# Kernel optimization log

Measured on AMD Instinct MI355X. Metric: run time of the kernel, lower is better.

## Reference

```python
import jax, jax.numpy as jnp
import numpy as np

D_IN, D_SAE, T, L, K = 2304, 2048, 4, 6, 128
B = 32


def setup_inputs() -> dict:
    key = jax.random.key(0)
    kx, ke, kd = jax.random.split(key, 3)
    x = jax.random.normal(kx, (B, T, L, D_IN), dtype=jnp.float32)
    W_enc = jax.random.normal(ke, (T, L, D_IN, D_SAE), dtype=jnp.float32) / np.sqrt(D_IN).astype(np.float32)
    W_dec = jax.random.normal(kd, (T, L, D_SAE, D_IN), dtype=jnp.float32) / np.sqrt(D_SAE).astype(np.float32)
    b_enc = jnp.zeros((D_SAE,), dtype=jnp.float32)
    b_dec = jnp.zeros((T, L, D_IN), dtype=jnp.float32)
    return {"x": x, "W_enc": W_enc, "W_dec": W_dec, "b_enc": b_enc, "b_dec": b_dec}


def reference(x, W_enc, W_dec, b_enc, b_dec):
    # encode: per-(t,l) matmul, pre: (B, T, L, d_sae)
    pre = jnp.einsum('btld,tlds->btls', x, W_enc) + b_enc
    Bn = pre.shape[0]
    pre_flat = pre.reshape(Bn, T * L * D_SAE)
    # global TopK over the whole (T, L, d_sae) latent grid
    v, idx = jax.lax.top_k(pre_flat, K)
    z_flat = jnp.zeros_like(pre_flat).at[jnp.arange(Bn)[:, None], idx].set(jax.nn.relu(v))
    z = z_flat.reshape(Bn, T, L, D_SAE)
    # decode: per-(t,l) matmul
    x_hat = jnp.einsum('btls,tlsd->btld', z, W_dec) + b_dec
    loss = jnp.mean(jnp.sum(jnp.square(x_hat - x), axis=-1))
    return (loss, x_hat, z)
```

## Files before the change

### kernel.cpp

```cpp
#include <hip/hip_runtime.h>

#define D_IN   2304
#define D_SAE  2048
#define TL     24
#define BATCH  32
#define K_TOP  128
#define NLAT   (TL * D_SAE)
#define NBIN   8192
#define CAP    2048
#define KSPLIT 2
#define KS     (D_IN / KSPLIT)
#define BK     32
#define NCH    (KS / BK)

typedef __attribute__((ext_vector_type(8))) short short8;
typedef __attribute__((ext_vector_type(4))) float f32x4;

__device__ __forceinline__ void async_cp16(const float* g, float* l) {
    __builtin_amdgcn_global_load_lds(
        (const __attribute__((address_space(1))) unsigned int*)g,
        (__attribute__((address_space(3))) unsigned int*)l, 16, 0, 0);
}

__device__ __forceinline__ void cvt8(const float* f, short8& hi, short8& lo) {
#pragma unroll
    for (int j = 0; j < 8; ++j) {
        unsigned u = __float_as_uint(f[j]);
        hi[j] = (short)(u >> 16);
        float l = f[j] - __uint_as_float(u & 0xFFFF0000u);
        lo[j] = (short)(__float_as_uint(l) >> 16);
    }
}

__global__ __launch_bounds__(256, 3) void enc_kernel(const float* __restrict__ x,
                                                     const float* __restrict__ W,
                                                     float* __restrict__ part) {
    __shared__ float w_s[2][BK][128];
    __shared__ float x_s[2][32][36];

    const int tid  = threadIdx.x;
    const int lane = tid & 63;
    const int wv   = tid >> 6;
    const int m0   = lane & 15;
    const int kb   = lane >> 4;
    const int tl   = blockIdx.y;
    const int ks   = blockIdx.z;
    const int n0b  = blockIdx.x * 128;
    const int kb0  = ks * KS;

    const float* Wbase = W + ((size_t)(tl * D_IN + kb0)) * D_SAE + n0b;
    const int xb = tid >> 3, xq = (tid & 7) * 4;
    const float* xsrc = x + ((size_t)(xb * TL + tl)) * D_IN + kb0 + xq;

#define STAGE_W(buf, ch)                                                        \
    do {                                                                        \
        const float* Wc = Wbase + (size_t)((ch) * BK) * D_SAE;                  \
        _Pragma("unroll")                                                       \
        for (int j = 0; j < 4; ++j) {                                           \
            int r = wv * 8 + j * 2;                                             \
            async_cp16(Wc + (size_t)(r + (lane >> 5)) * D_SAE + (lane & 31) * 4,\
                       &w_s[buf][r][0]);                                        \
        }                                                                       \
    } while (0)

    f32x4 acc[2][2];
#pragma unroll
    for (int mt = 0; mt < 2; ++mt)
#pragma unroll
        for (int nt = 0; nt < 2; ++nt) acc[mt][nt] = (f32x4)(0.f);

    {
        float4 xr = *(const float4*)xsrc;
        STAGE_W(0, 0);
        asm volatile("s_waitcnt vmcnt(0)" ::: "memory");
        *(float4*)&x_s[0][xb][xq] = xr;
        __syncthreads();
    }

    int cur = 0;
    for (int ch = 0; ch < NCH; ++ch) {
        float4 xr;
        if (ch + 1 < NCH) {
            xr = *(const float4*)(xsrc + (ch + 1) * BK);
            STAGE_W(cur ^ 1, ch + 1);
        }

        const float(*ws)[128] = w_s[cur];
        const float(*xs)[36]  = x_s[cur];
        short8 ahi[2], alo[2];
#pragma unroll
        for (int mt = 0; mt < 2; ++mt) {
            float xa[8];
            *(float4*)&xa[0] = *(const float4*)&xs[mt * 16 + m0][kb * 8];
            *(float4*)&xa[4] = *(const float4*)&xs[mt * 16 + m0][kb * 8 + 4];
            cvt8(xa, ahi[mt], alo[mt]);
        }
#pragma unroll
        for (int nt = 0; nt < 2; ++nt) {
            float wf[8];
#pragma unroll
            for (int j = 0; j < 8; ++j)
                wf[j] = ws[kb * 8 + j][wv * 32 + nt * 16 + m0];
            short8 bhi, blo;
            cvt8(wf, bhi, blo);
#pragma unroll
            for (int mt = 0; mt < 2; ++mt) {
                acc[mt][nt] = __builtin_amdgcn_mfma_f32_16x16x32_bf16(ahi[mt], bhi, acc[mt][nt], 0, 0, 0);
                acc[mt][nt] = __builtin_amdgcn_mfma_f32_16x16x32_bf16(ahi[mt], blo, acc[mt][nt], 0, 0, 0);
                acc[mt][nt] = __builtin_amdgcn_mfma_f32_16x16x32_bf16(alo[mt], bhi, acc[mt][nt], 0, 0, 0);
            }
        }

        if (ch + 1 < NCH) {
            asm volatile("s_waitcnt vmcnt(0)" ::: "memory");
            *(float4*)&x_s[cur ^ 1][xb][xq] = xr;
        }
        __syncthreads();
        cur ^= 1;
    }
#undef STAGE_W

    float* pp = part + ((size_t)ks * BATCH) * NLAT + (size_t)tl * D_SAE + n0b;
#pragma unroll
    for (int mt = 0; mt < 2; ++mt)
#pragma unroll
        for (int nt = 0; nt < 2; ++nt)
#pragma unroll
            for (int r = 0; r < 4; ++r)
                pp[(size_t)(mt * 16 + kb * 4 + r) * NLAT + wv * 32 + nt * 16 + m0] =
                    acc[mt][nt][r];
}

__global__ void reduce_kernel(const float* __restrict__ part,
                              const float* __restrict__ b_enc,
                              float* __restrict__ pre) {
    int i = (blockIdx.x * blockDim.x + threadIdx.x) * 4;
    const size_t S = (size_t)BATCH * NLAT;
    float4 v = *(const float4*)&b_enc[i & (D_SAE - 1)];
#pragma unroll
    for (int s = 0; s < KSPLIT; s++) {
        float4 p = *(const float4*)&part[i + s * S];
        v.x += p.x; v.y += p.y; v.z += p.z; v.w += p.w;
    }
    *(float4*)&pre[i] = v;
}

__global__ __launch_bounds__(256) void topk_kernel(const float* __restrict__ pre,
                                                   int* __restrict__ sel_idx,
                                                   float* __restrict__ sel_val,
                                                   float* __restrict__ z,
                                                   float* __restrict__ loss) {
    const int b   = blockIdx.x;
    const int tid = threadIdx.x;
    __shared__ unsigned hist[NBIN];
    __shared__ unsigned cand_key[CAP];
    __shared__ int      cand_idx[CAP];
    __shared__ unsigned tsum[256];
    __shared__ unsigned suf[256];
    __shared__ int s_T, s_hi, s_ccnt, s_sel;

    const float* row  = pre + (size_t)b * NLAT;
    float*       zrow = z   + (size_t)b * NLAT;
    for (int i = tid; i < NBIN; i += 256) hist[i] = 0;
    if (tid == 0) { s_ccnt = 0; s_sel = 0; if (b == 0) *loss = 0.f; }
    __syncthreads();

    for (int i = 4 * tid; i < NLAT; i += 1024) {
        float4 v = *(const float4*)&row[i];
#pragma unroll
        for (int j = 0; j < 4; j++) {
            unsigned u   = __float_as_uint(((const float*)&v)[j]);
            unsigned key = u ^ ((u >> 31) ? 0xFFFFFFFFu : 0x80000000u);
            atomicAdd(&hist[key >> 19], 1u);
        }
    }
    __syncthreads();

    unsigned local = 0;
    const int base = tid * (NBIN / 256);
    for (int j = 0; j < NBIN / 256; j++) local += hist[base + j];
    tsum[tid] = local;
    __syncthreads();
    if (tid == 0) {
        unsigned run = 0;
        for (int t = 255; t >= 0; t--) { suf[t] = run; run += tsum[t]; }
    }
    __syncthreads();
    if (suf[tid] < K_TOP && suf[tid] + tsum[tid] >= K_TOP) {
        unsigned c = suf[tid];
        for (int j = NBIN / 256 - 1; j >= 0; j--) {
            int bin = base + j;
            if (c + hist[bin] >= K_TOP) { s_T = bin; s_hi = (int)c; break; }
            c += hist[bin];
        }
    }
    __syncthreads();

    const int T = s_T;
    for (int i = 4 * tid; i < NLAT; i += 1024) {
        float4 v = *(const float4*)&row[i];
#pragma unroll
        for (int j = 0; j < 4; j++) {
            float f      = ((const float*)&v)[j];
            unsigned u   = __float_as_uint(f);
            unsigned key = u ^ ((u >> 31) ? 0xFFFFFFFFu : 0x80000000u);
            int bin      = (int)(key >> 19);
            float rl     = fmaxf(f, 0.f);
            float zval   = 0.f;
            if (bin > T) {
                int p = atomicAdd(&s_sel, 1);
                sel_idx[b * K_TOP + p] = i + j;
                sel_val[b * K_TOP + p] = rl;
                zval = rl;
            } else if (bin == T) {
                int p = atomicAdd(&s_ccnt, 1);
                if (p < CAP) { cand_key[p] = key; cand_idx[p] = i + j; }
            }
            zrow[i + j] = zval;
        }
    }
    __syncthreads();

    const int need = K_TOP - s_hi;
    const int nc   = min(s_ccnt, CAP);
    for (int c = tid; c < nc; c += 256) {
        unsigned kc = cand_key[c]; int ic = cand_idx[c];
        int rank = 0;
        for (int j = 0; j < nc; j++) {
            unsigned kj = cand_key[j]; int ij = cand_idx[j];
            rank += (kj > kc) || (kj == kc && ij < ic);
        }
        if (rank < need) {
            int p = atomicAdd(&s_sel, 1);
            float rl = fmaxf(row[ic], 0.f);
            sel_idx[b * K_TOP + p] = ic;
            sel_val[b * K_TOP + p] = rl;
            zrow[ic] = rl;
        }
    }
}

__global__ __launch_bounds__(256) void dec_kernel(const float* __restrict__ Wd,
                                                  const float* __restrict__ b_dec,
                                                  const float* __restrict__ x,
                                                  const int* __restrict__ sel_idx,
                                                  const float* __restrict__ sel_val,
                                                  float* __restrict__ xhat,
                                                  float* __restrict__ loss) {
    const int tl = blockIdx.x, b = blockIdx.y, tid = threadIdx.x;
    float acc[9];
#pragma unroll
    for (int r = 0; r < 9; r++) acc[r] = b_dec[tl * D_IN + tid + r * 256];

    __shared__ int   s_idx[K_TOP];
    __shared__ float s_val[K_TOP];
    if (tid < K_TOP) { s_idx[tid] = sel_idx[b * K_TOP + tid];
                       s_val[tid] = sel_val[b * K_TOP + tid]; }
    __syncthreads();

    for (int j = 0; j < K_TOP; j++) {
        int f = s_idx[j];
        if ((f >> 11) == tl) {
            float v = s_val[j];
            const float* wrow = Wd + (size_t)f * D_IN;
#pragma unroll
            for (int r = 0; r < 9; r++)
                acc[r] = fmaf(v, wrow[tid + r * 256], acc[r]);
        }
    }

    const float* xr = x    + ((size_t)b * TL + tl) * D_IN;
    float*       xo = xhat + ((size_t)b * TL + tl) * D_IN;
    float lsum = 0.f;
#pragma unroll
    for (int r = 0; r < 9; r++) {
        float d = acc[r] - xr[tid + r * 256];
        xo[tid + r * 256] = acc[r];
        lsum += d * d;
    }
    __shared__ float red[256];
    red[tid] = lsum; __syncthreads();
    for (int s = 128; s > 0; s >>= 1) {
        if (tid < s) red[tid] += red[tid + s];
        __syncthreads();
    }
    if (tid == 0) atomicAdd(loss, red[0] * (1.0f / (BATCH * TL)));
}

extern "C" void kernel_launch(void* const* d_in, const int* in_sizes, int n_in,
                              void* d_out, int out_size, void* d_ws, size_t ws_size,
                              hipStream_t stream) {
    const float* x     = (const float*)d_in[0];
    const float* W_enc = (const float*)d_in[1];
    const float* W_dec = (const float*)d_in[2];
    const float* b_enc = (const float*)d_in[3];
    const float* b_dec = (const float*)d_in[4];

    float* out  = (float*)d_out;
    float* loss = out;
    float* xhat = out + 1;
    float* z    = out + 1 + (size_t)BATCH * TL * D_IN;

    const size_t S = (size_t)BATCH * NLAT;
    float* part    = (float*)d_ws;
    float* pre     = part + (size_t)KSPLIT * S;
    int*   sel_idx = (int*)(pre + S);
    float* sel_val = (float*)(sel_idx + BATCH * K_TOP);

    enc_kernel<<<dim3(16, TL, KSPLIT), 256, 0, stream>>>(x, W_enc, part);
    reduce_kernel<<<(int)(S / 1024), 256, 0, stream>>>(part, b_enc, pre);
    topk_kernel<<<BATCH, 256, 0, stream>>>(pre, sel_idx, sel_val, z, loss);
    dec_kernel<<<dim3(TL, BATCH), 256, 0, stream>>>(W_dec, b_dec, x, sel_idx, sel_val,
                                                    xhat, loss);
}
```

Baseline: 167.2 us.

## Pre-transpose x, async-stage both operands, and move top-k histogram into reduce pass

Adds a transpose kernel that writes x in a swizzled per-(t,l) layout and also zeroes a global histogram and the loss. The encoder now loads both operands with async global-to-LDS copies, using XOR-swizzled columns to avoid bank conflicts, and its occupancy hint rises to 4. The reduce kernel now zeros z and builds per-row histograms with global atomics, so the top-k kernel skips one full pass over each row. Top-k runs with 512 threads and a parallel suffix scan instead of a serial one. The costs are an extra launch, extra workspace, and heavy global atomic contention on the histogram bins.

```diff
diff --git a/kernel.cpp b/kernel.cpp
--- a/kernel.cpp
+++ b/kernel.cpp
@@ -12,6 +12,7 @@
 #define KS     (D_IN / KSPLIT)
 #define BK     32
 #define NCH    (KS / BK)
+#define TOPK_T 512
 
 typedef __attribute__((ext_vector_type(8))) short short8;
 typedef __attribute__((ext_vector_type(4))) float f32x4;
@@ -32,11 +33,35 @@
     }
 }
 
-__global__ __launch_bounds__(256, 3) void enc_kernel(const float* __restrict__ x,
+__global__ __launch_bounds__(256) void xT_kernel(const float* __restrict__ x,
+                                                 float* __restrict__ xT,
+                                                 unsigned* __restrict__ ghist,
+                                                 float* __restrict__ loss) {
+    __shared__ float ts[32][257];
+    const int tl = blockIdx.y, k0 = blockIdx.x * 256, tid = threadIdx.x;
+#pragma unroll 4
+    for (int r = 0; r < 32; ++r)
+        ts[r][tid] = x[((size_t)(r * TL + tl)) * D_IN + k0 + tid];
+    __syncthreads();
+    const int bb = tid & 31, kq = tid >> 5;
+#pragma unroll 4
+    for (int jj = 0; jj < 32; ++jj) {
+        int kk = kq + jj * 8;
+        int kg = k0 + kk;
+        int pc = (bb + 8 * ((kg >> 3) & 3)) & 31;
+        xT[((size_t)tl * D_IN + kg) * 32 + pc] = ts[bb][kk];
+    }
+    int gid = (blockIdx.y * gridDim.x + blockIdx.x) * 256 + tid;
+    for (int i = gid; i < BATCH * NBIN / 4; i += 216 * 256)
+        ((uint4*)ghist)[i] = make_uint4(0, 0, 0, 0);
+    if (gid == 0) *loss = 0.f;
+}
+
+__global__ __launch_bounds__(256, 4) void enc_kernel(const float* __restrict__ xT,
                                                      const float* __restrict__ W,
                                                      float* __restrict__ part) {
     __shared__ float w_s[2][BK][128];
-    __shared__ float x_s[2][32][36];
+    __shared__ float x_s[2][BK][32];
 
     const int tid  = threadIdx.x;
     const int lane = tid & 63;
@@ -45,22 +70,28 @@
     const int kb   = lane >> 4;
     const int tl   = blockIdx.y;
     const int ks   = blockIdx.z;
-    const int n0b  = blockIdx.x * 128;
-    const int kb0  = ks * KS;
-
-    const float* Wbase = W + ((size_t)(tl * D_IN + kb0)) * D_SAE + n0b;
-    const int xb = tid >> 3, xq = (tid & 7) * 4;
-    const float* xsrc = x + ((size_t)(xb * TL + tl)) * D_IN + kb0 + xq;
-
-#define STAGE_W(buf, ch)                                                        \
+    const int col0 = blockIdx.x * 128;
+
+    const float* Wbase = W + ((size_t)(tl * D_IN + ks * KS)) * D_SAE + col0;
+    const float* xbase = xT + ((size_t)(tl * D_IN + ks * KS)) * 32;
+
+    int colp[2];
+#pragma unroll
+    for (int nt = 0; nt < 2; ++nt)
+        colp[nt] = ((((wv * 8 + nt * 4 + (m0 >> 2)) ^ kb)) << 2) | (m0 & 3);
+    const int c0 = (m0 + 8 * kb) & 31;
+    const int c1 = (m0 + 16 + 8 * kb) & 31;
+
+#define STAGE(BUF, CH)                                                          \
     do {                                                                        \
-        const float* Wc = Wbase + (size_t)((ch) * BK) * D_SAE;                  \
+        const float* Wc = Wbase + (size_t)(CH) * BK * D_SAE;                    \
         _Pragma("unroll")                                                       \
-        for (int j = 0; j < 4; ++j) {                                           \
-            int r = wv * 8 + j * 2;                                             \
-            async_cp16(Wc + (size_t)(r + (lane >> 5)) * D_SAE + (lane & 31) * 4,\
-                       &w_s[buf][r][0]);                                        \
-        }                                                                       \
+        for (int i = 0; i < 4; ++i)                                             \
+            async_cp16(Wc + (size_t)(wv * 8 + 2 * i + (lane >> 5)) * D_SAE      \
+                          + ((lane & 31) ^ wv) * 4,                             \
+                       &w_s[BUF][wv * 8 + 2 * i][0]);                           \
+        async_cp16(xbase + (CH) * 1024 + wv * 256 + lane * 4,                   \
+                   &x_s[BUF][wv * 8][0]);                                       \
     } while (0)
 
     f32x4 acc[2][2];
@@ -69,58 +100,48 @@
 #pragma unroll
         for (int nt = 0; nt < 2; ++nt) acc[mt][nt] = (f32x4)(0.f);
 
-    {
-        float4 xr = *(const float4*)xsrc;
-        STAGE_W(0, 0);
-        asm volatile("s_waitcnt vmcnt(0)" ::: "memory");
-        *(float4*)&x_s[0][xb][xq] = xr;
-        __syncthreads();
-    }
+    STAGE(0, 0);
+    asm volatile("s_waitcnt vmcnt(0)" ::: "memory");
+    __builtin_amdgcn_s_barrier();
 
     int cur = 0;
     for (int ch = 0; ch < NCH; ++ch) {
-        float4 xr;
-        if (ch + 1 < NCH) {
-            xr = *(const float4*)(xsrc + (ch + 1) * BK);
-            STAGE_W(cur ^ 1, ch + 1);
-        }
+        if (ch + 1 < NCH) STAGE(cur ^ 1, ch + 1);
 
         const float(*ws)[128] = w_s[cur];
-        const float(*xs)[36]  = x_s[cur];
-        short8 ahi[2], alo[2];
-#pragma unroll
-        for (int mt = 0; mt < 2; ++mt) {
+        const float(*xs)[32]  = x_s[cur];
+        short8 a0h, a0l, a1h, a1l;
+        {
             float xa[8];
-            *(float4*)&xa[0] = *(const float4*)&xs[mt * 16 + m0][kb * 8];
-            *(float4*)&xa[4] = *(const float4*)&xs[mt * 16 + m0][kb * 8 + 4];
-            cvt8(xa, ahi[mt], alo[mt]);
+#pragma unroll
+            for (int j = 0; j < 8; ++j) xa[j] = xs[kb * 8 + j][c0];
+            cvt8(xa, a0h, a0l);
+#pragma unroll
+            for (int j = 0; j < 8; ++j) xa[j] = xs[kb * 8 + j][c1];
+            cvt8(xa, a1h, a1l);
         }
 #pragma unroll
         for (int nt = 0; nt < 2; ++nt) {
             float wf[8];
 #pragma unroll
-            for (int j = 0; j < 8; ++j)
-                wf[j] = ws[kb * 8 + j][wv * 32 + nt * 16 + m0];
+            for (int j = 0; j < 8; ++j) wf[j] = ws[kb * 8 + j][colp[nt]];
             short8 bhi, blo;
             cvt8(wf, bhi, blo);
-#pragma unroll
-            for (int mt = 0; mt < 2; ++mt) {
-                acc[mt][nt] = __builtin_amdgcn_mfma_f32_16x16x32_bf16(ahi[mt], bhi, acc[mt][nt], 0, 0, 0);
-                acc[mt][nt] = __builtin_amdgcn_mfma_f32_16x16x32_bf16(ahi[mt], blo, acc[mt][nt], 0, 0, 0);
-                acc[mt][nt] = __builtin_amdgcn_mfma_f32_16x16x32_bf16(alo[mt], bhi, acc[mt][nt], 0, 0, 0);
-            }
-        }
-
-        if (ch + 1 < NCH) {
-            asm volatile("s_waitcnt vmcnt(0)" ::: "memory");
-            *(float4*)&x_s[cur ^ 1][xb][xq] = xr;
-        }
-        __syncthreads();
+            acc[0][nt] = __builtin_amdgcn_mfma_f32_16x16x32_bf16(a0h, bhi, acc[0][nt], 0, 0, 0);
+            acc[0][nt] = __builtin_amdgcn_mfma_f32_16x16x32_bf16(a0h, blo, acc[0][nt], 0, 0, 0);
+            acc[0][nt] = __builtin_amdgcn_mfma_f32_16x16x32_bf16(a0l, bhi, acc[0][nt], 0, 0, 0);
+            acc[1][nt] = __builtin_amdgcn_mfma_f32_16x16x32_bf16(a1h, bhi, acc[1][nt], 0, 0, 0);
+            acc[1][nt] = __builtin_amdgcn_mfma_f32_16x16x32_bf16(a1h, blo, acc[1][nt], 0, 0, 0);
+            acc[1][nt] = __builtin_amdgcn_mfma_f32_16x16x32_bf16(a1l, bhi, acc[1][nt], 0, 0, 0);
+        }
+
+        asm volatile("s_waitcnt vmcnt(0)" ::: "memory");
+        __builtin_amdgcn_s_barrier();
         cur ^= 1;
     }
-#undef STAGE_W
-
-    float* pp = part + ((size_t)ks * BATCH) * NLAT + (size_t)tl * D_SAE + n0b;
+#undef STAGE
+
+    float* pp = part + ((size_t)ks * BATCH) * NLAT + (size_t)tl * D_SAE + col0;
 #pragma unroll
     for (int mt = 0; mt < 2; ++mt)
 #pragma unroll
@@ -131,64 +152,68 @@
                     acc[mt][nt][r];
 }
 
-__global__ void reduce_kernel(const float* __restrict__ part,
-                              const float* __restrict__ b_enc,
-                              float* __restrict__ pre) {
-    int i = (blockIdx.x * blockDim.x + threadIdx.x) * 4;
+__global__ __launch_bounds__(256) void reduce_hist_kernel(const float* __restrict__ part,
+                                                          const float* __restrict__ b_enc,
+                                                          float* __restrict__ pre,
+                                                          float* __restrict__ z,
+                                                          unsigned* __restrict__ ghist) {
+    int i = (blockIdx.x * 256 + threadIdx.x) * 4;
     const size_t S = (size_t)BATCH * NLAT;
+    const int b = i / NLAT;
     float4 v = *(const float4*)&b_enc[i & (D_SAE - 1)];
 #pragma unroll
-    for (int s = 0; s < KSPLIT; s++) {
+    for (int s = 0; s < KSPLIT; ++s) {
         float4 p = *(const float4*)&part[i + s * S];
         v.x += p.x; v.y += p.y; v.z += p.z; v.w += p.w;
     }
     *(float4*)&pre[i] = v;
-}
-
-__global__ __launch_bounds__(256) void topk_kernel(const float* __restrict__ pre,
-                                                   int* __restrict__ sel_idx,
-                                                   float* __restrict__ sel_val,
-                                                   float* __restrict__ z,
-                                                   float* __restrict__ loss) {
+    z[i] = 0.f; z[i + 1] = 0.f; z[i + 2] = 0.f; z[i + 3] = 0.f;
+#pragma unroll
+    for (int j = 0; j < 4; ++j) {
+        unsigned u   = __float_as_uint(((const float*)&v)[j]);
+        unsigned key = u ^ ((u >> 31) ? 0xFFFFFFFFu : 0x80000000u);
+        atomicAdd(&ghist[b * NBIN + (key >> 19)], 1u);
+    }
+}
+
+__global__ __launch_bounds__(TOPK_T) void topk_kernel(const float* __restrict__ pre,
+                                                      const unsigned* __restrict__ ghist,
+                                                      int* __restrict__ sel_idx,
+                                                      float* __restrict__ sel_val,
+                                                      float* __restrict__ z) {
     const int b   = blockIdx.x;
     const int tid = threadIdx.x;
     __shared__ unsigned hist[NBIN];
     __shared__ unsigned cand_key[CAP];
     __shared__ int      cand_idx[CAP];
-    __shared__ unsigned tsum[256];
-    __shared__ unsigned suf[256];
+    __shared__ unsigned tsum[TOPK_T];
+    __shared__ unsigned scan[TOPK_T];
     __shared__ int s_T, s_hi, s_ccnt, s_sel;
 
     const float* row  = pre + (size_t)b * NLAT;
     float*       zrow = z   + (size_t)b * NLAT;
-    for (int i = tid; i < NBIN; i += 256) hist[i] = 0;
-    if (tid == 0) { s_ccnt = 0; s_sel = 0; if (b == 0) *loss = 0.f; }
-    __syncthreads();
-
-    for (int i = 4 * tid; i < NLAT; i += 1024) {
-        float4 v = *(const float4*)&row[i];
-#pragma unroll
-        for (int j = 0; j < 4; j++) {
-            unsigned u   = __float_as_uint(((const float*)&v)[j]);
-            unsigned key = u ^ ((u >> 31) ? 0xFFFFFFFFu : 0x80000000u);
-            atomicAdd(&hist[key >> 19], 1u);
-        }
-    }
+    for (int i = tid; i < NBIN; i += TOPK_T)
+        hist[i] = ghist[b * NBIN + i];
+    if (tid == 0) { s_ccnt = 0; s_sel = 0; }
     __syncthreads();
 
     unsigned local = 0;
-    const int base = tid * (NBIN / 256);
-    for (int j = 0; j < NBIN / 256; j++) local += hist[base + j];
+    const int base = tid * (NBIN / TOPK_T);
+#pragma unroll
+    for (int j = 0; j < NBIN / TOPK_T; j++) local += hist[base + j];
     tsum[tid] = local;
-    __syncthreads();
-    if (tid == 0) {
-        unsigned run = 0;
-        for (int t = 255; t >= 0; t--) { suf[t] = run; run += tsum[t]; }
-    }
-    __syncthreads();
-    if (suf[tid] < K_TOP && suf[tid] + tsum[tid] >= K_TOP) {
-        unsigned c = suf[tid];
-        for (int j = NBIN / 256 - 1; j >= 0; j--) {
+    scan[tid] = local;
+    __syncthreads();
+    for (int d = 1; d < TOPK_T; d <<= 1) {
+        unsigned v = scan[tid] + ((tid + d < TOPK_T) ? scan[tid + d] : 0u);
+        __syncthreads();
+        scan[tid] = v;
+        __syncthreads();
+    }
+    const unsigned suf_e = scan[tid] - tsum[tid];
+    if (suf_e < K_TOP && suf_e + tsum[tid] >= K_TOP) {
+        unsigned c = suf_e;
+        for (int j = NBIN / TOPK_T - 1; j >= 0; j--) {
             int bin = base + j;
             if (c + hist[bin] >= K_TOP) { s_T = bin; s_hi = (int)c; break; }
             c += hist[bin];
@@ -197,7 +222,7 @@
     __syncthreads();
 
     const int T = s_T;
-    for (int i = 4 * tid; i < NLAT; i += 1024) {
+    for (int i = 4 * tid; i < NLAT; i += 4 * TOPK_T) {
         float4 v = *(const float4*)&row[i];
 #pragma unroll
         for (int j = 0; j < 4; j++) {
@@ -205,25 +230,23 @@
             unsigned u   = __float_as_uint(f);
             unsigned key = u ^ ((u >> 31) ? 0xFFFFFFFFu : 0x80000000u);
             int bin      = (int)(key >> 19);
-            float rl     = fmaxf(f, 0.f);
-            float zval   = 0.f;
             if (bin > T) {
                 int p = atomicAdd(&s_sel, 1);
+                float rl = fmaxf(f, 0.f);
                 sel_idx[b * K_TOP + p] = i + j;
                 sel_val[b * K_TOP + p] = rl;
-                zval = rl;
+                zrow[i + j] = rl;
             } else if (bin == T) {
                 int p = atomicAdd(&s_ccnt, 1);
                 if (p < CAP) { cand_key[p] = key; cand_idx[p] = i + j; }
             }
-            zrow[i + j] = zval;
         }
     }
     __syncthreads();
 
     const int need = K_TOP - s_hi;
     const int nc   = min(s_ccnt, CAP);
-    for (int c = tid; c < nc; c += 256) {
+    for (int c = tid; c < nc; c += TOPK_T) {
         unsigned kc = cand_key[c]; int ic = cand_idx[c];
         int rank = 0;
         for (int j = 0; j < nc; j++) {
@@ -302,14 +325,17 @@
     float* z    = out + 1 + (size_t)BATCH * TL * D_IN;
 
     const size_t S = (size_t)BATCH * NLAT;
-    float* part    = (float*)d_ws;
-    float* pre     = part + (size_t)KSPLIT * S;
-    int*   sel_idx = (int*)(pre + S);
-    float* sel_val = (float*)(sel_idx + BATCH * K_TOP);
-
-    enc_kernel<<<dim3(16, TL, KSPLIT), 256, 0, stream>>>(x, W_enc, part);
-    reduce_kernel<<<(int)(S / 1024), 256, 0, stream>>>(part, b_enc, pre);
-    topk_kernel<<<BATCH, 256, 0, stream>>>(pre, sel_idx, sel_val, z, loss);
+    float*    part    = (float*)d_ws;
+    float*    pre     = part + (size_t)KSPLIT * S;
+    float*    xT      = pre + S;
+    unsigned* ghist   = (unsigned*)(xT + (size_t)TL * D_IN * 32);
+    int*      sel_idx = (int*)(ghist + (size_t)BATCH * NBIN);
+    float*    sel_val = (float*)(sel_idx + BATCH * K_TOP);
+
+    xT_kernel<<<dim3(D_IN / 256, TL), 256, 0, stream>>>(x, xT, ghist, loss);
+    enc_kernel<<<dim3(16, TL, KSPLIT), 256, 0, stream>>>(xT, W_enc, part);
+    reduce_hist_kernel<<<(int)(S / 1024), 256, 0, stream>>>(part, b_enc, pre, z, ghist);
+    topk_kernel<<<BATCH, TOPK_T, 0, stream>>>(pre, ghist, sel_idx, sel_val, z);
     dec_kernel<<<dim3(TL, BATCH), 256, 0, stream>>>(W_dec, b_dec, x, sel_idx, sel_val,
                                                     xhat, loss);
 }
```

New measurement: 260.7 us. 1.56x slower.
